# Kernel optimization log

Hardware: AMD Instinct MI355X
Metric: run time of the kernel (lower is better)

## Reference

```python
import jax, jax.numpy as jnp
import numpy as np
from jax import lax

NUM_GROUPS = 16
GN_EPS = 1e-5
POOL = 4
CLAMP_MIN, CLAMP_MAX = 0.0, 1.0


def setup_inputs() -> dict:
    key = jax.random.key(0)
    ks = jax.random.split(key, 4)
    x = jax.random.normal(ks[0], (128, 8, 128, 128), dtype=jnp.float32)
    conv_weight = jax.random.normal(ks[1], (64, 8, 3, 3), dtype=jnp.float32) * 0.1
    conv_bias = jax.random.normal(ks[2], (64,), dtype=jnp.float32) * 0.1
    gn_weight = jnp.ones((64,), dtype=jnp.float32)
    gn_bias = jnp.zeros((64,), dtype=jnp.float32)
    scale = jax.random.normal(ks[3], (64, 1, 1), dtype=jnp.float32)
    return {"x": x, "conv_weight": conv_weight, "conv_bias": conv_bias,
            "gn_weight": gn_weight, "gn_bias": gn_bias, "scale": scale}


def reference(x, conv_weight, conv_bias, gn_weight, gn_bias, scale):
    # Conv2d (stride=1, padding=0)
    y = lax.conv_general_dilated(
        x, conv_weight, window_strides=(1, 1), padding='VALID',
        dimension_numbers=('NCHW', 'OIHW', 'NCHW'))
    y = y + conv_bias[None, :, None, None]  # [B, C, H, W] = [128, 64, 126, 126]

    # GroupNorm over (channels-in-group, H, W) per sample
    B, C, H, W = y.shape
    yg = y.reshape(B, NUM_GROUPS, C // NUM_GROUPS, H, W)
    mean = jnp.mean(yg, axis=(2, 3, 4), keepdims=True)
    var = jnp.var(yg, axis=(2, 3, 4), keepdims=True)
    yn = ((yg - mean) * lax.rsqrt(var + GN_EPS)).reshape(B, C, H, W)
    yn = yn * gn_weight[None, :, None, None] + gn_bias[None, :, None, None]

    # scale (broadcast [C,1,1])
    yn = yn * scale[None]

    # MaxPool2d(kernel=4, stride=4)
    p = lax.reduce_window(yn, -jnp.inf, lax.max,
                          window_dimensions=(1, 1, POOL, POOL),
                          window_strides=(1, 1, POOL, POOL),
                          padding='VALID')  # [128, 64, 31, 31]

    # clamp
    return jnp.clip(p, CLAMP_MIN, CLAMP_MAX)
```

## Files before the change

kernel.cpp:

```cpp
#include <hip/hip_runtime.h>
#include <math.h>

typedef _Float16 f16x8 __attribute__((ext_vector_type(8)));
typedef float f32x4 __attribute__((ext_vector_type(4)));

#define CIN 8
#define HIN 128
#define WIN 128
#define OH 126
#define OW 126
#define COUT 64
#define NB 128
#define NGROUPS 16
#define CPG 4
#define PWN 31
#define XROWS 34
#define XH_DIM 130
#define TPIX (34*34)
#define XSPAD 3072

#define XH_BYTES   ((size_t)NB*XH_DIM*XH_DIM*CIN*2)
#define WEXT_BYTES ((size_t)NB*PWN*PWN*COUT*2)
#define PART_BYTES ((size_t)NB*NGROUPS*4*2*4)
#define WH_BYTES   ((size_t)9*64*8*2)
#define WS_NEEDED  (XH_BYTES + WEXT_BYTES + PART_BYTES + WH_BYTES)

#define NPOOL (NB*PWN*PWN*COUT)
#define OFF_PART_OLD (NPOOL/2)

__global__ __launch_bounds__(192)
void xpack_kernel(const float* __restrict__ x, const float* __restrict__ w,
                  _Float16* __restrict__ xh, _Float16* __restrict__ wh)
{
  const int iy = blockIdx.x;
  const int b  = blockIdx.y;
  if (iy == XH_DIM) {
    if (b != 0) return;
    for (int i = threadIdx.x; i < 9*64*8; i += 192) {
      const int khw = i >> 9, rem = i & 511;
      wh[i] = (_Float16)w[rem*9 + khw];
    }
    return;
  }
  const int ix = threadIdx.x;
  if (ix >= XH_DIM) return;
  f16x8 pk = {0,0,0,0,0,0,0,0};
  if (iy < HIN && ix < WIN) {
    const float* xb = x + (size_t)b*CIN*HIN*WIN + iy*WIN + ix;
    #pragma unroll
    for (int ci = 0; ci < 8; ++ci)
      pk[ci] = (_Float16)xb[ci*HIN*WIN];
  }
  *(f16x8*)&xh[(((size_t)b*XH_DIM + iy)*XH_DIM + ix)*CIN] = pk;
}

__global__ __launch_bounds__(512)
void conv_dma_kernel(const _Float16* __restrict__ xh,
                     const _Float16* __restrict__ wh,
                     const float* __restrict__ bias,
                     const float* __restrict__ gnw,
                     const float* __restrict__ scale,
                     _Float16* __restrict__ wext,
                     float* __restrict__ parts)
{
  __shared__ __align__(16) _Float16 xs[2][TPIX*8 + XSPAD];
  __shared__ __align__(8)  _Float16 sbuf[8][256];
  __shared__ float red[8][16][2];

  const int tid  = threadIdx.x;
  const int lane = tid & 63, wv = tid >> 6;
  const int tx = blockIdx.x;
  const int b  = blockIdx.y;
  const int ox0 = tx*32;

  const int q = lane >> 4, ln = lane & 15;

  auto stage = [&](int buf, int ty) {
    const int oy0 = ty*32;
    #pragma unroll
    for (int k = 0; k < 3; ++k) {
      const int p = k*512 + tid;
      if (p < TPIX) {
        const int r = p / 34, c = p - r*34;
        const size_t gb = (((size_t)b*XH_DIM + (oy0 + r))*XH_DIM + (ox0 + c))*CIN;
        __builtin_amdgcn_global_load_lds(
            (const __attribute__((address_space(1))) void*)(xh + gb),
            (__attribute__((address_space(3))) void*)&xs[buf][p*8],
            16, 0, 0);
      }
    }
  };

  stage(0, 0);

  f16x8 bf[4][3];
  #pragma unroll
  for (int nt = 0; nt < 4; ++nt) {
    #pragma unroll
    for (int c = 0; c < 2; ++c)
      bf[nt][c] = *(const f16x8*)&wh[((c*4 + q)*64 + nt*16 + ln)*8];
    if (q == 0)
      bf[nt][2] = *(const f16x8*)&wh[((8)*64 + nt*16 + ln)*8];
    else
      bf[nt][2] = (f16x8){0,0,0,0,0,0,0,0};
  }

  int aoff[3];
  #pragma unroll
  for (int c = 0; c < 3; ++c) {
    const int khw = c*4 + q;
    const int ky = khw / 3, kx = khw - 3*(khw/3);
    aoff[c] = (khw < 9) ? (ky*34 + kx + ln)*8 : ln*8;
  }

  float bias_r[4], sgn[4];
  #pragma unroll
  for (int nt = 0; nt < 4; ++nt) {
    const int c = nt*16 + ln;
    bias_r[nt] = bias[c];
    sgn[nt] = (gnw[c]*scale[c] >= 0.f) ? 1.f : -1.f;
  }

  float s[4]  = {0.f,0.f,0.f,0.f};
  float sq[4] = {0.f,0.f,0.f,0.f};

  const float xm_hi = (q < 3) ? 1.f : 0.f;

  asm volatile("s_waitcnt vmcnt(0)" ::: "memory");
  __syncthreads();

  for (int ty = 0; ty < 4; ++ty) {
    const int cur = ty & 1;
    if (ty < 3) stage(cur ^ 1, ty + 1);

    const int wy_g = ty*8 + wv;
    const int oy0  = ty*32;

    #pragma unroll
    for (int bd = 0; bd < 2; ++bd) {
      const int x0 = bd << 4;
      const bool xedge = (tx == 3) && (bd == 1);

      float mx[4] = {-1e30f, -1e30f, -1e30f, -1e30f};

      #pragma unroll
      for (int sy = 0; sy < 4; ++sy) {
        const int y_l = wv*4 + sy;
        if (oy0 + y_l >= OH) break;
        const int base = (y_l*34 + x0)*8;

        f32x4 acc[4];
        #pragma unroll
        for (int nt = 0; nt < 4; ++nt) {
          const float bv = bias_r[nt];
          acc[nt] = (f32x4){bv, bv, bv, bv};
        }
        #pragma unroll
        for (int c = 0; c < 3; ++c) {
          const f16x8 a = *(const f16x8*)&xs[cur][base + aoff[c]];
          #pragma unroll
          for (int nt = 0; nt < 4; ++nt)
            acc[nt] = __builtin_amdgcn_mfma_f32_16x16x32_f16(a, bf[nt][c], acc[nt], 0, 0, 0);
        }

        #pragma unroll
        for (int nt = 0; nt < 4; ++nt) {
          float v0 = acc[nt][0], v1 = acc[nt][1];
          float v2 = acc[nt][2], v3 = acc[nt][3];
          if (xedge) { v2 *= xm_hi; v3 *= xm_hi; }
          s[nt]  += (v0+v1) + (v2+v3);
          sq[nt] += v0*v0 + v1*v1 + v2*v2 + v3*v3;
          const float sg = sgn[nt];
          const float m = fmaxf(fmaxf(sg*v0, sg*v1), fmaxf(sg*v2, sg*v3));
          mx[nt] = fmaxf(mx[nt], m);
        }
      }

      if (wy_g < PWN) {
        #pragma unroll
        for (int nt = 0; nt < 4; ++nt)
          sbuf[wv][q*64 + nt*16 + ln] = (_Float16)(sgn[nt]*mx[nt]);
        const int nw = xedge ? 3 : 4;
        if (lane < nw*16) {
          const int wx0_g = tx*8 + (x0 >> 2);
          const uint2 v = *(const uint2*)&sbuf[wv][lane*4];
          *(uint2*)&wext[(((size_t)b*PWN + wy_g)*PWN + wx0_g)*COUT + lane*4] = v;
        }
      }
    }

    if (ty < 3) {
      asm volatile("s_waitcnt vmcnt(0)" ::: "memory");
      __syncthreads();
    }
  }

  #pragma unroll
  for (int nt = 0; nt < 4; ++nt) {
    float a = s[nt], c2 = sq[nt];
    a  += __shfl_xor(a, 16, 64);  a  += __shfl_xor(a, 32, 64);
    a  += __shfl_xor(a, 1, 64);   a  += __shfl_xor(a, 2, 64);
    c2 += __shfl_xor(c2, 16, 64); c2 += __shfl_xor(c2, 32, 64);
    c2 += __shfl_xor(c2, 1, 64);  c2 += __shfl_xor(c2, 2, 64);
    if (lane < 16 && (lane & 3) == 0) {
      red[wv][nt*4 + (ln >> 2)][0] = a;
      red[wv][nt*4 + (ln >> 2)][1] = c2;
    }
  }
  __syncthreads();
  if (tid < 32) {
    const int g = tid >> 1, k = tid & 1;
    float t = 0.f;
    #pragma unroll
    for (int w8 = 0; w8 < 8; ++w8) t += red[w8][g][k];
    parts[(((size_t)b*NGROUPS + g)*4 + tx)*2 + k] = t;
  }
}

__global__ __launch_bounds__(256)
void conv_mfma_kernel(const float* __restrict__ x,
                      const float* __restrict__ w,
                      const float* __restrict__ bias,
                      const float* __restrict__ gnw,
                      const float* __restrict__ scale,
                      float* __restrict__ ws)
{
  __shared__ __align__(16) _Float16 xs[XROWS*34*8];
  __shared__ __align__(16) _Float16 wls[9*64*8];
  __shared__ float red[4][16][2];

  const int tid  = threadIdx.x;
  const int lane = tid & 63, wave = tid >> 6;
  const int tileIdx = blockIdx.x;
  const int tx = tileIdx & 3, ty = tileIdx >> 2;
  const int b  = blockIdx.y;
  const int ox0 = tx*32, oy0 = ty*32;

  for (int idx = tid; idx < 9*64*8; idx += 256) {
    const int ci = idx & 7, n = (idx >> 3) & 63, khw = idx >> 9;
    wls[idx] = (_Float16)w[(n*CIN + ci)*9 + khw];
  }
  const float* xb = x + (size_t)b * CIN*HIN*WIN;
  for (int p = tid; p < XROWS*34; p += 256) {
    const int r = p / 34, c = p - r*34;
    const int iy = oy0 + r, ix = ox0 + c;
    const bool ok = (iy < HIN) && (ix < WIN);
    const int gbase = iy*WIN + ix;
    f16x8 pk;
    #pragma unroll
    for (int ci = 0; ci < 8; ++ci) {
      const float v = ok ? xb[ci*HIN*WIN + gbase] : 0.f;
      pk[ci] = (_Float16)v;
    }
    *(f16x8*)&xs[p*8] = pk;
  }
  __syncthreads();

  const int q = lane >> 4, ln = lane & 15;
  f16x8 bf[4][3];
  #pragma unroll
  for (int nt = 0; nt < 4; ++nt) {
    #pragma unroll
    for (int c = 0; c < 2; ++c)
      bf[nt][c] = *(const f16x8*)&wls[((c*4 + q)*64 + nt*16 + ln)*8];
    if (q == 0) bf[nt][2] = *(const f16x8*)&wls[((8)*64 + nt*16 + ln)*8];
    else        bf[nt][2] = (f16x8){0,0,0,0,0,0,0,0};
  }
  const int dy = ln >> 2, dx = ln & 3;
  int aoff[3];
  #pragma unroll
  for (int c = 0; c < 3; ++c) {
    const int khw = c*4 + q;
    const int ky = khw / 3, kx = khw - 3*(khw/3);
    aoff[c] = (khw < 9) ? ((dy + ky)*34 + (dx + kx))*8 : 0;
  }
  float bias_r[4], sgn[4];
  #pragma unroll
  for (int nt = 0; nt < 4; ++nt) {
    const int c = nt*16 + ln;
    bias_r[nt] = bias[c];
    sgn[nt] = (gnw[c]*scale[c] >= 0.f) ? 1.f : -1.f;
  }
  float s[4]  = {0.f,0.f,0.f,0.f};
  float sq[4] = {0.f,0.f,0.f,0.f};
  _Float16* wext = (_Float16*)ws;

  #pragma unroll 2
  for (int i = 0; i < 16; ++i) {
    const int wyl = wave*2 + (i >> 3), wxl = i & 7;
    const int base = (wyl*4*34 + wxl*4)*8;
    f32x4 acc[4];
    #pragma unroll
    for (int nt = 0; nt < 4; ++nt) {
      const float bv = bias_r[nt];
      acc[nt] = (f32x4){bv, bv, bv, bv};
    }
    #pragma unroll
    for (int c = 0; c < 3; ++c) {
      const f16x8 a = *(const f16x8*)&xs[base + aoff[c]];
      #pragma unroll
      for (int nt = 0; nt < 4; ++nt)
        acc[nt] = __builtin_amdgcn_mfma_f32_16x16x32_f16(a, bf[nt][c], acc[nt], 0, 0, 0);
    }
    const int wyg = ty*8 + wyl, wxg = tx*8 + wxl;
    if ((wyg < PWN) && (wxg < PWN)) {
      const size_t rowbase = ((size_t)(b*PWN + wyg)*PWN + wxg)*COUT;
      float m4[4];
      #pragma unroll
      for (int nt = 0; nt < 4; ++nt) {
        const float v0 = acc[nt][0], v1 = acc[nt][1];
        const float v2 = acc[nt][2], v3 = acc[nt][3];
        s[nt]  += (v0+v1) + (v2+v3);
        sq[nt] += v0*v0 + v1*v1 + v2*v2 + v3*v3;
        const float sg = sgn[nt];
        float m = fmaxf(fmaxf(sg*v0, sg*v1), fmaxf(sg*v2, sg*v3));
        m = fmaxf(m, __shfl_xor(m, 16, 64));
        m = fmaxf(m, __shfl_xor(m, 32, 64));
        m4[nt] = sg*m;
      }
      float mv = m4[0];
      mv = (q == 1) ? m4[1] : mv;
      mv = (q == 2) ? m4[2] : mv;
      mv = (q == 3) ? m4[3] : mv;
      wext[rowbase + lane] = (_Float16)mv;
    } else {
      const bool yv = (wyg*4 + q) < OH;
      #pragma unroll
      for (int nt = 0; nt < 4; ++nt) {
        #pragma unroll
        for (int r = 0; r < 4; ++r) {
          const bool okp = yv && (wxg*4 + r < OW);
          const float v = okp ? acc[nt][r] : 0.f;
          s[nt] += v; sq[nt] += v*v;
        }
      }
    }
  }
  #pragma unroll
  for (int nt = 0; nt < 4; ++nt) {
    float a = s[nt], c2 = sq[nt];
    a  += __shfl_xor(a, 16, 64);  a  += __shfl_xor(a, 32, 64);
    a  += __shfl_xor(a, 1, 64);   a  += __shfl_xor(a, 2, 64);
    c2 += __shfl_xor(c2, 16, 64); c2 += __shfl_xor(c2, 32, 64);
    c2 += __shfl_xor(c2, 1, 64);  c2 += __shfl_xor(c2, 2, 64);
    if (lane < 16 && (lane & 3) == 0) {
      red[wave][nt*4 + (ln >> 2)][0] = a;
      red[wave][nt*4 + (ln >> 2)][1] = c2;
    }
  }
  __syncthreads();
  if (tid < 32) {
    const int g = tid >> 1, k = tid & 1;
    const float t = red[0][g][k] + red[1][g][k] + red[2][g][k] + red[3][g][k];
    ws[OFF_PART_OLD + (((size_t)b*NGROUPS + g)*16 + tileIdx)*2 + k] = t;
  }
}

__global__ __launch_bounds__(256)
void tail_kernel(const float* __restrict__ gnw,
                 const float* __restrict__ gnb,
                 const float* __restrict__ scale,
                 const _Float16* __restrict__ wext,
                 const float* __restrict__ parts,
                 const int nparts,
                 float* __restrict__ out)
{
  __shared__ float stat[NGROUPS*2];
  __shared__ float AB[128];
  __shared__ float vout[COUT*PWN];

  const int tid = threadIdx.x;
  const int xb  = blockIdx.x;
  const int b   = blockIdx.y;

  if (tid < 32) {
    const int g = tid >> 1, k = tid & 1;
    const float* p = parts + ((size_t)(b*NGROUPS + g)*nparts)*2 + k;
    float a = 0.f;
    for (int t = 0; t < nparts; ++t) a += p[t*2];
    stat[g*2 + k] = a;
  }
  __syncthreads();
  if (tid < COUT) {
    const int c = tid, g = c >> 2;
    const float N = (float)(CPG * OH * OW);
    const float mean = stat[g*2] / N;
    const float var  = stat[g*2 + 1] / N - mean*mean;
    const float inv  = rsqrtf(var + 1e-5f);
    const float ag   = inv * gnw[c];
    AB[c]      = ag * scale[c];
    AB[64 + c] = (gnb[c] - mean * ag) * scale[c];
  }
  __syncthreads();

  #pragma unroll
  for (int r = 0; r < 2; ++r) {
    const int wy = xb*2 + r;
    if (wy >= PWN) break;
    const size_t rb = (size_t)(b*PWN + wy)*PWN*COUT;

    if (tid < 248) {
      const f16x8 e = *(const f16x8*)&wext[rb + tid*8];
      const int wx = tid >> 3, c0 = (tid & 7)*8;
      #pragma unroll
      for (int j = 0; j < 8; ++j) {
        const int c = c0 + j;
        float v = fmaf(AB[c], (float)e[j], AB[64 + c]);
        v = fminf(fmaxf(v, 0.f), 1.f);
        vout[c*PWN + wx] = v;
      }
    }
    __syncthreads();
    for (int e = tid; e < COUT*PWN; e += 256) {
      const int c = e / PWN, wx = e - c*PWN;
      out[(((size_t)b*COUT + c)*PWN + wy)*PWN + wx] = vout[e];
    }
    __syncthreads();
  }
}

extern "C" void kernel_launch(void* const* d_in, const int* in_sizes, int n_in,
                              void* d_out, int out_size, void* d_ws, size_t ws_size,
                              hipStream_t stream)
{
  const float* x     = (const float*)d_in[0];
  const float* cw    = (const float*)d_in[1];
  const float* cb    = (const float*)d_in[2];
  const float* gnw   = (const float*)d_in[3];
  const float* gnb   = (const float*)d_in[4];
  const float* scale = (const float*)d_in[5];
  float* out = (float*)d_out;
  float* ws  = (float*)d_ws;

  if (ws_size >= WS_NEEDED) {
    _Float16* xh   = (_Float16*)ws;
    _Float16* wext = (_Float16*)((char*)ws + XH_BYTES);
    float*    prt  = (float*)((char*)ws + XH_BYTES + WEXT_BYTES);
    _Float16* wh   = (_Float16*)((char*)ws + XH_BYTES + WEXT_BYTES + PART_BYTES);

    xpack_kernel<<<dim3(XH_DIM + 1, NB), 192, 0, stream>>>(x, cw, xh, wh);
    conv_dma_kernel<<<dim3(4, NB), 512, 0, stream>>>(xh, wh, cb, gnw, scale, wext, prt);
    tail_kernel<<<dim3(16, NB), 256, 0, stream>>>(gnw, gnb, scale, wext, prt, 4, out);
  } else {
    conv_mfma_kernel<<<dim3(16, NB), 256, 0, stream>>>(x, cw, cb, gnw, scale, ws);
    tail_kernel<<<dim3(16, NB), 256, 0, stream>>>(gnw, gnb, scale,
                                                  (const _Float16*)ws,
                                                  ws + OFF_PART_OLD, 16, out);
  }
}
```

Measured before the change: 167.2 us.

## Fuse input fp16 packing and weight conversion into conv kernel

```diff
diff --git a/kernel.cpp b/kernel.cpp
--- a/kernel.cpp
+++ b/kernel.cpp
@@ -22,46 +22,20 @@
 #define XH_BYTES   ((size_t)NB*XH_DIM*XH_DIM*CIN*2)
 #define WEXT_BYTES ((size_t)NB*PWN*PWN*COUT*2)
 #define PART_BYTES ((size_t)NB*NGROUPS*4*2*4)
-#define WH_BYTES   ((size_t)9*64*8*2)
-#define WS_NEEDED  (XH_BYTES + WEXT_BYTES + PART_BYTES + WH_BYTES)
+#define WS_NEEDED  (XH_BYTES + WEXT_BYTES + PART_BYTES)
 
 #define NPOOL (NB*PWN*PWN*COUT)
 #define OFF_PART_OLD (NPOOL/2)
 
-__global__ __launch_bounds__(192)
-void xpack_kernel(const float* __restrict__ x, const float* __restrict__ w,
-                  _Float16* __restrict__ xh, _Float16* __restrict__ wh)
-{
-  const int iy = blockIdx.x;
-  const int b  = blockIdx.y;
-  if (iy == XH_DIM) {
-    if (b != 0) return;
-    for (int i = threadIdx.x; i < 9*64*8; i += 192) {
-      const int khw = i >> 9, rem = i & 511;
-      wh[i] = (_Float16)w[rem*9 + khw];
-    }
-    return;
-  }
-  const int ix = threadIdx.x;
-  if (ix >= XH_DIM) return;
-  f16x8 pk = {0,0,0,0,0,0,0,0};
-  if (iy < HIN && ix < WIN) {
-    const float* xb = x + (size_t)b*CIN*HIN*WIN + iy*WIN + ix;
-    #pragma unroll
-    for (int ci = 0; ci < 8; ++ci)
-      pk[ci] = (_Float16)xb[ci*HIN*WIN];
-  }
-  *(f16x8*)&xh[(((size_t)b*XH_DIM + iy)*XH_DIM + ix)*CIN] = pk;
-}
-
 __global__ __launch_bounds__(512)
-void conv_dma_kernel(const _Float16* __restrict__ xh,
-                     const _Float16* __restrict__ wh,
-                     const float* __restrict__ bias,
-                     const float* __restrict__ gnw,
-                     const float* __restrict__ scale,
-                     _Float16* __restrict__ wext,
-                     float* __restrict__ parts)
+void conv_fused_kernel(const float* __restrict__ x,
+                       const float* __restrict__ w,
+                       const float* __restrict__ bias,
+                       const float* __restrict__ gnw,
+                       const float* __restrict__ scale,
+                       _Float16* __restrict__ xh,
+                       _Float16* __restrict__ wext,
+                       float* __restrict__ parts)
 {
   __shared__ __align__(16) _Float16 xs[2][TPIX*8 + XSPAD];
   __shared__ __align__(8)  _Float16 sbuf[8][256];
@@ -72,8 +46,24 @@
   const int tx = blockIdx.x;
   const int b  = blockIdx.y;
   const int ox0 = tx*32;
-
   const int q = lane >> 4, ln = lane & 15;
+
+  const float* xb = x + (size_t)b * CIN*HIN*WIN;
+  auto packchunk = [&](int T) {
+    const int y0 = T*32;
+    for (int p = tid; p < TPIX; p += 512) {
+      const int r = p / 34, c = p - r*34;
+      const int iy = y0 + r, ix = ox0 + c;
+      f16x8 pk = {0,0,0,0,0,0,0,0};
+      if (iy < HIN && ix < WIN) {
+        const int gb = iy*WIN + ix;
+        #pragma unroll
+        for (int ci = 0; ci < 8; ++ci)
+          pk[ci] = (_Float16)xb[ci*HIN*WIN + gb];
+      }
+      *(f16x8*)&xh[(((size_t)b*XH_DIM + iy)*XH_DIM + ix)*CIN] = pk;
+    }
+  };
 
   auto stage = [&](int buf, int ty) {
     const int oy0 = ty*32;
@@ -91,18 +81,27 @@
     }
   };
 
-  stage(0, 0);
+  packchunk(0);
+  packchunk(1);
 
   f16x8 bf[4][3];
   #pragma unroll
   for (int nt = 0; nt < 4; ++nt) {
-    #pragma unroll
-    for (int c = 0; c < 2; ++c)
-      bf[nt][c] = *(const f16x8*)&wh[((c*4 + q)*64 + nt*16 + ln)*8];
-    if (q == 0)
-      bf[nt][2] = *(const f16x8*)&wh[((8)*64 + nt*16 + ln)*8];
-    else
+    const int n = nt*16 + ln;
+    #pragma unroll
+    for (int c = 0; c < 2; ++c) {
+      const int khw = c*4 + q;
+      #pragma unroll
+      for (int ci = 0; ci < 8; ++ci)
+        bf[nt][c][ci] = (_Float16)w[(n*CIN + ci)*9 + khw];
+    }
+    if (q == 0) {
+      #pragma unroll
+      for (int ci = 0; ci < 8; ++ci)
+        bf[nt][2][ci] = (_Float16)w[(n*CIN + ci)*9 + 8];
+    } else {
       bf[nt][2] = (f16x8){0,0,0,0,0,0,0,0};
+    }
   }
 
   int aoff[3];
@@ -128,10 +127,14 @@
 
   asm volatile("s_waitcnt vmcnt(0)" ::: "memory");
   __syncthreads();
+  stage(0, 0);
+  asm volatile("s_waitcnt vmcnt(0)" ::: "memory");
+  __syncthreads();
 
   for (int ty = 0; ty < 4; ++ty) {
     const int cur = ty & 1;
     if (ty < 3) stage(cur ^ 1, ty + 1);
+    if (ty < 2) packchunk(ty + 2);
 
     const int wy_g = ty*8 + wv;
     const int oy0  = ty*32;
@@ -436,10 +439,8 @@
     _Float16* xh   = (_Float16*)ws;
     _Float16* wext = (_Float16*)((char*)ws + XH_BYTES);
     float*    prt  = (float*)((char*)ws + XH_BYTES + WEXT_BYTES);
-    _Float16* wh   = (_Float16*)((char*)ws + XH_BYTES + WEXT_BYTES + PART_BYTES);
-
-    xpack_kernel<<<dim3(XH_DIM + 1, NB), 192, 0, stream>>>(x, cw, xh, wh);
-    conv_dma_kernel<<<dim3(4, NB), 512, 0, stream>>>(xh, wh, cb, gnw, scale, wext, prt);
+
+    conv_fused_kernel<<<dim3(4, NB), 512, 0, stream>>>(x, cw, cb, gnw, scale, xh, wext, prt);
     tail_kernel<<<dim3(16, NB), 256, 0, stream>>>(gnw, gnb, scale, wext, prt, 4, out);
   } else {
     conv_mfma_kernel<<<dim3(16, NB), 256, 0, stream>>>(x, cw, cb, gnw, scale, ws);
```

Measured after the change: 204.3 us. 22.1% more time.
